# Kernel optimization log

Hardware: AMD Instinct MI355X
Metric: run time of the kernel (lower is better)

The kernel has to match this reference:

```python
import jax, jax.numpy as jnp
import numpy as np


def setup_inputs() -> dict:
    key = jax.random.key(0)
    kq, kk, kv = jax.random.split(key, 3)
    B, Lq, Lk, D = 4, 4096, 4096, 64
    return {
        "Q": jax.random.normal(kq, (B, Lq, D), dtype=jnp.float32),
        "K": jax.random.normal(kk, (B, Lk, D), dtype=jnp.float32),
        "V": jax.random.normal(kv, (B, Lk, D), dtype=jnp.float32),
    }


def reference(Q, K, V):
    # scores: [B, Lq, Lk]  (no 1/sqrt(d) scaling in the original module)
    scores = jnp.einsum("bqd,bkd->bqk", Q, K)
    attn = jax.nn.softmax(scores, axis=-1)
    # output: [B, Lq, D]
    return jnp.einsum("bqk,bkd->bqd", attn, V)
```

## Files before the change

### kernel.cpp

```cpp
#include <hip/hip_runtime.h>
#include <cmath>


#define B_    4
#define LQ    4096
#define LK    4096
#define DH    64
#define BQ    128
#define NQT2  (B_ * LQ / BQ)
#define NKVT  (LK / 128)
#define NROWS (B_ * LQ)
#define LOG2E 1.44269504088896f
#define C0    63.4785817991f

typedef _Float16 f16x8 __attribute__((ext_vector_type(8)));
typedef _Float16 f16x4 __attribute__((ext_vector_type(4)));
typedef float    f32x4 __attribute__((ext_vector_type(4)));
typedef short    s16x8 __attribute__((ext_vector_type(8)));
typedef int      i32x4 __attribute__((ext_vector_type(4)));

__device__ inline float exp2_(float x) {
#if __has_builtin(__builtin_amdgcn_exp2f)
  return __builtin_amdgcn_exp2f(x);
#else
  return exp2f(x);
#endif
}

__device__ inline unsigned pkbf16(float lo, float hi) {
  return __builtin_amdgcn_perm(__float_as_uint(hi), __float_as_uint(lo),
                               0x07060302u);
}

__device__ inline unsigned short bf16rne(float f) {
  unsigned u = __float_as_uint(f);
  return (unsigned short)((u + 0x7FFF + ((u >> 16) & 1)) >> 16);
}

__device__ inline void async16(const void* g, void* l) {
  __builtin_amdgcn_global_load_lds(
      (const __attribute__((address_space(1))) unsigned int*)g,
      (__attribute__((address_space(3))) unsigned int*)l, 16, 0, 0);
}

__global__ __launch_bounds__(256) void convert_kv8(
    const float* __restrict__ K, const float* __restrict__ V,
    const float* __restrict__ Q, _Float16* __restrict__ Kh,
    unsigned short* __restrict__ Vb, _Float16* __restrict__ Qh) {
  __shared__ unsigned short Vs[64 * 68];
  const int tid = threadIdx.x;
  const int bb = blockIdx.x;

  if (bb < 256) {
    const int b = bb >> 6, tile = (bb >> 1) & 31, half = bb & 1;
    const int kv0 = tile * 128 + half * 64;
    for (int i = 0; i < 2; ++i) {
      int q = i * 256 + tid;
      int r = q >> 3, g = q & 7;
      const float* src = K + ((size_t)(b * LK + kv0 + r)) * DH + g * 8;
      float4 a = *(const float4*)src;
      float4 d = *(const float4*)(src + 4);
      f16x8 hv = {(_Float16)(a.x * LOG2E), (_Float16)(a.y * LOG2E),
                  (_Float16)(a.z * LOG2E), (_Float16)(a.w * LOG2E),
                  (_Float16)(d.x * LOG2E), (_Float16)(d.y * LOG2E),
                  (_Float16)(d.z * LOG2E), (_Float16)(d.w * LOG2E)};
      int gp = g ^ (r & 7);
      size_t dst = ((size_t)(b * 32 + tile) * 128 + half * 64 + r) * 64 + gp * 8;
      *(f16x8*)(&Kh[dst]) = hv;
    }
  } else if (bb < 512) {
    const int cc = bb - 256;
    const int b = cc >> 6, tile = (cc >> 1) & 31, half = cc & 1;
    const int kv0 = tile * 128 + half * 64;
    for (int i = 0; i < 4; ++i) {
      int idx = i * 256 + tid;
      int vr = idx >> 4, c4 = idx & 15;
      float4 v = *(const float4*)(&V[((size_t)(b * LK + kv0 + vr)) * DH + c4 * 4]);
      Vs[vr * 68 + c4 * 4 + 0] = bf16rne(v.x);
      Vs[vr * 68 + c4 * 4 + 1] = bf16rne(v.y);
      Vs[vr * 68 + c4 * 4 + 2] = bf16rne(v.z);
      Vs[vr * 68 + c4 * 4 + 3] = bf16rne(v.w);
    }
    __syncthreads();
    for (int i = 0; i < 2; ++i) {
      int q = i * 256 + tid;
      int d = q >> 3, gl = q & 7;
      int g = half * 8 + gl;
      unsigned short ov[8];
#pragma unroll
      for (int j = 0; j < 8; ++j) {
        int p = g * 8 + j;
        int c = p >> 5, w5 = p & 31;
        int qd = w5 >> 3, jj = w5 & 7, hh = jj >> 2, r = jj & 3;
        int sL = 32 * c + 16 * hh + 4 * qd + r - 64 * half;
        ov[j] = Vs[sL * 68 + d];
      }
      int gp = g ^ (d & 7);
      size_t dst = ((size_t)(b * 32 + tile) * 64 + d) * 128 + gp * 8;
      s16x8 o8;
#pragma unroll
      for (int j = 0; j < 8; ++j) o8[j] = (short)ov[j];
      *(s16x8*)(&Vb[dst]) = o8;
    }
  } else {
    const int u = bb - 512;
    for (int i = 0; i < 4; ++i) {
      int idx = i * 256 + tid;
      int r = idx >> 4, c4 = idx & 15;
      size_t off = ((size_t)u * 64 + r) * DH + c4 * 4;
      float4 v = *(const float4*)(&Q[off]);
      f16x4 h = {(_Float16)v.x, (_Float16)v.y, (_Float16)v.z, (_Float16)v.w};
      *(f16x4*)(&Qh[off]) = h;
    }
  }
}

__global__ __launch_bounds__(256, 4) void ca_flash8(
    const _Float16* __restrict__ Qh, const _Float16* __restrict__ Kh,
    const unsigned short* __restrict__ Vb, float* __restrict__ Out,
    _Float16* __restrict__ Opart, float* __restrict__ Lw, int nsplit) {
  __shared__ _Float16 KsH[128 * 64];
  __shared__ unsigned short VtH[64 * 128];

  const int tid  = threadIdx.x;
  const int wave = tid >> 6;
  const int lane = tid & 63;
  const int quad = lane >> 4;
  const int l16  = lane & 15;
  const int e    = quad ^ (l16 & 7);

  const int qt    = blockIdx.x;
  const int b     = qt >> 5;
  const int qbase = (qt & 31) * BQ;
  const int sp    = blockIdx.y;
  const int t0 = (NKVT * sp) / nsplit;
  const int t1 = (NKVT * (sp + 1)) / nsplit;

  f16x8 qf[2][2];
#pragma unroll
  for (int sub = 0; sub < 2; ++sub) {
    int qrow = qbase + wave * 32 + sub * 16 + l16;
    const _Float16* qp = Qh + ((size_t)b * LQ + qrow) * DH + quad * 8;
#pragma unroll
    for (int kk = 0; kk < 2; ++kk)
      qf[sub][kk] = *(const f16x8*)(qp + kk * 32);
  }

  f32x4 o[2][5];
#pragma unroll
  for (int sub = 0; sub < 2; ++sub)
#pragma unroll
    for (int td = 0; td < 5; ++td) o[sub][td] = (f32x4){0.f, 0.f, 0.f, 0.f};

  s16x8 ones;
#pragma unroll
  for (int j = 0; j < 8; ++j) ones[j] = (short)0x3F80;

  const char* kg = (const char*)Kh + ((size_t)(b * 32 + t0)) * 16384;
  const char* vg = (const char*)Vb + ((size_t)(b * 32 + t0)) * 16384;
  char* ksB = (char*)KsH;
  char* vtB = (char*)VtH;
  const char* kR = ksB + l16 * 128;
  const char* vR = vtB + l16 * 256;

  for (int tile = t0; tile < t1; ++tile) {
    __syncthreads();
    const char* sg = (wave < 2) ? (kg + wave * 8192) : (vg + (wave - 2) * 8192);
    char*       sd = (wave < 2) ? (ksB + wave * 8192) : (vtB + (wave - 2) * 8192);
#pragma unroll
    for (int i = 0; i < 8; ++i) async16(sg + i * 1024 + lane * 16, sd + i * 1024);
    __syncthreads();
    kg += 16384; vg += 16384;

#pragma unroll
    for (int c = 0; c < 4; ++c) {
      f32x4 sv[2][2];
#pragma unroll
      for (int sub = 0; sub < 2; ++sub)
#pragma unroll
        for (int tt = 0; tt < 2; ++tt)
          sv[sub][tt] = (f32x4){-C0, -C0, -C0, -C0};
#pragma unroll
      for (int kk = 0; kk < 2; ++kk) {
        int ko = (e ^ (4 * kk)) * 16;
#pragma unroll
        for (int tt = 0; tt < 2; ++tt) {
          f16x8 bk = *(const f16x8*)(kR + (2 * c + tt) * 2048 + ko);
          sv[0][tt] = __builtin_amdgcn_mfma_f32_16x16x32_f16(bk, qf[0][kk], sv[0][tt], 0, 0, 0);
          sv[1][tt] = __builtin_amdgcn_mfma_f32_16x16x32_f16(bk, qf[1][kk], sv[1][tt], 0, 0, 0);
        }
      }

      s16x8 ap[2];
#pragma unroll
      for (int sub = 0; sub < 2; ++sub) {
        unsigned u0 = pkbf16(exp2_(sv[sub][0][0]), exp2_(sv[sub][0][1]));
        unsigned u1 = pkbf16(exp2_(sv[sub][0][2]), exp2_(sv[sub][0][3]));
        unsigned u2 = pkbf16(exp2_(sv[sub][1][0]), exp2_(sv[sub][1][1]));
        unsigned u3 = pkbf16(exp2_(sv[sub][1][2]), exp2_(sv[sub][1][3]));
        i32x4 iv = {(int)u0, (int)u1, (int)u2, (int)u3};
        ap[sub] = __builtin_bit_cast(s16x8, iv);
      }

      int vo = (e ^ (4 * c)) * 16;
#pragma unroll
      for (int td = 0; td < 4; ++td) {
        s16x8 bv = *(const s16x8*)(vR + td * 4096 + vo);
        o[0][td] = __builtin_amdgcn_mfma_f32_16x16x32_bf16(ap[0], bv, o[0][td], 0, 0, 0);
        o[1][td] = __builtin_amdgcn_mfma_f32_16x16x32_bf16(ap[1], bv, o[1][td], 0, 0, 0);
      }
      o[0][4] = __builtin_amdgcn_mfma_f32_16x16x32_bf16(ap[0], ones, o[0][4], 0, 0, 0);
      o[1][4] = __builtin_amdgcn_mfma_f32_16x16x32_bf16(ap[1], ones, o[1][4], 0, 0, 0);
    }
  }

  if (nsplit == 1) {
#pragma unroll
    for (int sub = 0; sub < 2; ++sub)
#pragma unroll
      for (int r = 0; r < 4; ++r) {
        float inv = 1.0f / (o[sub][4][r] + 1e-35f);
        size_t row = (size_t)b * LQ + qbase + wave * 32 + sub * 16 + quad * 4 + r;
#pragma unroll
        for (int td = 0; td < 4; ++td)
          Out[row * DH + td * 16 + l16] = o[sub][td][r] * inv;
      }
    return;
  }

#pragma unroll
  for (int sub = 0; sub < 2; ++sub)
#pragma unroll
    for (int r = 0; r < 4; ++r) {
      float l = o[sub][4][r];
      float inv = 1.0f / (l + 1e-35f);
      size_t g = (size_t)qt * BQ + wave * 32 + sub * 16 + quad * 4 + r;
      size_t prow = (size_t)sp * NROWS + g;
#pragma unroll
      for (int td = 0; td < 4; ++td)
        Opart[prow * DH + td * 16 + l16] = (_Float16)(o[sub][td][r] * inv);
      if (l16 == 0) Lw[prow] = l;
    }
}

__global__ __launch_bounds__(256) void ca_combine8(
    const _Float16* __restrict__ Opart, const float* __restrict__ Lw,
    float* __restrict__ Out, int nsplit) {
  const int idx = blockIdx.x * 256 + threadIdx.x;
  const int g = idx >> 4;
  const int c0 = (idx & 15) * 4;
  float den = 1e-30f;
  float a0 = 0.f, a1 = 0.f, a2 = 0.f, a3 = 0.f;
  for (int s = 0; s < nsplit; ++s) {
    size_t prow = (size_t)s * NROWS + g;
    float w = Lw[prow];
    f16x4 v = *(const f16x4*)(&Opart[prow * DH + c0]);
    a0 += w * (float)v[0]; a1 += w * (float)v[1];
    a2 += w * (float)v[2]; a3 += w * (float)v[3];
    den += w;
  }
  float inv = 1.0f / den;
  float4 ov = {a0 * inv, a1 * inv, a2 * inv, a3 * inv};
  *(float4*)(&Out[(size_t)g * DH + c0]) = ov;
}

#define LDSS 72
__global__ __launch_bounds__(256) void ca_flash_naive(
    const float* __restrict__ Q, const float* __restrict__ K,
    const float* __restrict__ V, float* __restrict__ Out) {
  __shared__ _Float16 Qs[64 * LDSS];
  __shared__ _Float16 Ks[64 * LDSS];
  __shared__ _Float16 Vt[64 * LDSS];
  __shared__ _Float16 Ps[64 * LDSS];
  const int tid = threadIdx.x, wave = tid >> 6, lane = tid & 63;
  const int quad = lane >> 4, l16 = lane & 15;
  const int b = blockIdx.x >> 6, qbase = (blockIdx.x & 63) * 64;
  for (int i = 0; i < 4; ++i) {
    int idx = (i * 256 + tid) * 4;
    int r = idx >> 6, c = idx & 63;
    float4 q4 = *(const float4*)(&Q[((size_t)b * LQ + qbase + r) * DH + c]);
    f16x4 hh = {(_Float16)q4.x, (_Float16)q4.y, (_Float16)q4.z, (_Float16)q4.w};
    *(f16x4*)(&Qs[r * LDSS + c]) = hh;
  }
  __syncthreads();
  f16x8 qf[2];
  qf[0] = *(const f16x8*)(&Qs[(wave * 16 + l16) * LDSS + quad * 8]);
  qf[1] = *(const f16x8*)(&Qs[(wave * 16 + l16) * LDSS + quad * 8 + 32]);
  float m_i[4], l_i[4];
  f32x4 o[4];
  for (int r = 0; r < 4; ++r) {
    m_i[r] = -INFINITY; l_i[r] = 0.f; o[r] = (f32x4){0.f, 0.f, 0.f, 0.f};
  }
  for (int kv0 = 0; kv0 < LK; kv0 += 64) {
    __syncthreads();
    for (int i = 0; i < 4; ++i) {
      int idx = (i * 256 + tid) * 4;
      int r = idx >> 6, c = idx & 63;
      float4 k4 = *(const float4*)(&K[((size_t)b * LK + kv0 + r) * DH + c]);
      f16x4 hh = {(_Float16)k4.x, (_Float16)k4.y, (_Float16)k4.z, (_Float16)k4.w};
      *(f16x4*)(&Ks[r * LDSS + c]) = hh;
      float4 v4 = *(const float4*)(&V[((size_t)b * LK + kv0 + r) * DH + c]);
      Vt[(c + 0) * LDSS + r] = (_Float16)v4.x;
      Vt[(c + 1) * LDSS + r] = (_Float16)v4.y;
      Vt[(c + 2) * LDSS + r] = (_Float16)v4.z;
      Vt[(c + 3) * LDSS + r] = (_Float16)v4.w;
    }
    __syncthreads();
    f32x4 sv[4];
    for (int t = 0; t < 4; ++t) sv[t] = (f32x4){0.f, 0.f, 0.f, 0.f};
    for (int kk = 0; kk < 2; ++kk)
      for (int t = 0; t < 4; ++t) {
        f16x8 bk = *(const f16x8*)(&Ks[(t * 16 + l16) * LDSS + quad * 8 + kk * 32]);
        sv[t] = __builtin_amdgcn_mfma_f32_16x16x32_f16(qf[kk], bk, sv[t], 0, 0, 0);
      }
    for (int r = 0; r < 4; ++r) {
      float mx = fmaxf(fmaxf(sv[0][r], sv[1][r]), fmaxf(sv[2][r], sv[3][r]));
      for (int off = 1; off < 16; off <<= 1) mx = fmaxf(mx, __shfl_xor(mx, off, 64));
      float mnew = fmaxf(m_i[r], mx);
      float alpha = __expf(m_i[r] - mnew);
      float rs = 0.f;
      for (int t = 0; t < 4; ++t) { float p = __expf(sv[t][r] - mnew); sv[t][r] = p; rs += p; }
      for (int off = 1; off < 16; off <<= 1) rs += __shfl_xor(rs, off, 64);
      l_i[r] = l_i[r] * alpha + rs;
      m_i[r] = mnew;
      for (int td = 0; td < 4; ++td) o[td][r] *= alpha;
    }
    for (int t = 0; t < 4; ++t)
      for (int r = 0; r < 4; ++r)
        Ps[(wave * 16 + quad * 4 + r) * LDSS + t * 16 + l16] = (_Float16)sv[t][r];
    for (int kk = 0; kk < 2; ++kk) {
      f16x8 ap = *(const f16x8*)(&Ps[(wave * 16 + l16) * LDSS + quad * 8 + kk * 32]);
      for (int td = 0; td < 4; ++td) {
        f16x8 bv = *(const f16x8*)(&Vt[(td * 16 + l16) * LDSS + quad * 8 + kk * 32]);
        o[td] = __builtin_amdgcn_mfma_f32_16x16x32_f16(ap, bv, o[td], 0, 0, 0);
      }
    }
  }
  float inv_l[4];
  for (int r = 0; r < 4; ++r) inv_l[r] = 1.0f / l_i[r];
  for (int td = 0; td < 4; ++td)
    for (int r = 0; r < 4; ++r) {
      size_t row = (size_t)b * LQ + qbase + wave * 16 + quad * 4 + r;
      Out[row * DH + td * 16 + l16] = o[td][r] * inv_l[r];
    }
}

extern "C" void kernel_launch(void* const* d_in, const int* in_sizes, int n_in,
                              void* d_out, int out_size, void* d_ws, size_t ws_size,
                              hipStream_t stream) {
  const float* Q = (const float*)d_in[0];
  const float* K = (const float*)d_in[1];
  const float* V = (const float*)d_in[2];
  float* Out = (float*)d_out;

  const size_t sKh = (size_t)B_ * LK * DH * sizeof(_Float16);
  const size_t sVb = (size_t)B_ * LK * DH * sizeof(unsigned short);
  const size_t sQh = (size_t)NROWS * DH * sizeof(_Float16);
  const size_t base = sKh + sVb + sQh;
  auto opSize = [](int sp) { return (size_t)sp * NROWS * DH * sizeof(_Float16); };
  auto lwSize = [](int sp) { return (size_t)sp * NROWS * sizeof(float); };

  int split = 0;
  if (base + opSize(8) + lwSize(8) <= ws_size) split = 8;
  else if (base + opSize(4) + lwSize(4) <= ws_size) split = 4;
  else if (base + opSize(2) + lwSize(2) <= ws_size) split = 2;
  else if (base <= ws_size) split = 1;

  char* ws = (char*)d_ws;
  if (split >= 1) {
    _Float16* Kh = (_Float16*)ws;
    unsigned short* Vb = (unsigned short*)(ws + sKh);
    _Float16* Qh = (_Float16*)(ws + sKh + sVb);
    convert_kv8<<<dim3(768), dim3(256), 0, stream>>>(K, V, Q, Kh, Vb, Qh);
    if (split == 1) {
      ca_flash8<<<dim3(NQT2, 1), dim3(256), 0, stream>>>(
          Qh, Kh, Vb, Out, nullptr, nullptr, 1);
    } else {
      _Float16* Op = (_Float16*)(ws + base);
      float* Lwp = (float*)(ws + base + opSize(split));
      ca_flash8<<<dim3(NQT2, split), dim3(256), 0, stream>>>(
          Qh, Kh, Vb, Out, Op, Lwp, split);
      ca_combine8<<<dim3(NROWS * DH / 4 / 256), dim3(256), 0, stream>>>(
          Op, Lwp, Out, split);
    }
  } else {
    ca_flash_naive<<<dim3(256), dim3(256), 0, stream>>>(Q, K, V, Out);
  }
}
```

Baseline: 94.02 us.

## Double query tile per block to 256 rows for more K/V reuse

Each wave now handles 64 query rows (four 16-row sub-tiles) instead of 32, so every K/V tile staged in LDS feeds twice as many MFMAs. This halves the global-to-LDS traffic and the barrier count per query row. The cost is roughly double the accumulator and Q-fragment registers, with the occupancy hint lowered from 4 to 2 blocks per CU. With split 8 the grid shrinks from 1024 to 512 blocks, which may underfill the GPU.

Result: no change. 95.08 us (+1.1%).

```diff
diff --git a/kernel.cpp b/kernel.cpp
--- a/kernel.cpp
+++ b/kernel.cpp
@@ -6,8 +6,8 @@
 #define LQ    4096
 #define LK    4096
 #define DH    64
-#define BQ    128
-#define NQT2  (B_ * LQ / BQ)
+#define BQ    256
+#define NQT3  (B_ * LQ / BQ)
 #define NKVT  (LK / 128)
 #define NROWS (B_ * LQ)
 #define LOG2E 1.44269504088896f
@@ -115,7 +115,7 @@
   }
 }
 
-__global__ __launch_bounds__(256, 4) void ca_flash8(
+__global__ __launch_bounds__(256, 2) void ca_flash9(
     const _Float16* __restrict__ Qh, const _Float16* __restrict__ Kh,
     const unsigned short* __restrict__ Vb, float* __restrict__ Out,
     _Float16* __restrict__ Opart, float* __restrict__ Lw, int nsplit) {
@@ -130,25 +130,25 @@
   const int e    = quad ^ (l16 & 7);
 
   const int qt    = blockIdx.x;
-  const int b     = qt >> 5;
-  const int qbase = (qt & 31) * BQ;
+  const int b     = qt >> 4;
+  const int qbase = (qt & 15) * BQ;
   const int sp    = blockIdx.y;
   const int t0 = (NKVT * sp) / nsplit;
   const int t1 = (NKVT * (sp + 1)) / nsplit;
 
-  f16x8 qf[2][2];
-#pragma unroll
-  for (int sub = 0; sub < 2; ++sub) {
-    int qrow = qbase + wave * 32 + sub * 16 + l16;
+  f16x8 qf[4][2];
+#pragma unroll
+  for (int sub = 0; sub < 4; ++sub) {
+    int qrow = qbase + wave * 64 + sub * 16 + l16;
     const _Float16* qp = Qh + ((size_t)b * LQ + qrow) * DH + quad * 8;
 #pragma unroll
     for (int kk = 0; kk < 2; ++kk)
       qf[sub][kk] = *(const f16x8*)(qp + kk * 32);
   }
 
-  f32x4 o[2][5];
-#pragma unroll
-  for (int sub = 0; sub < 2; ++sub)
+  f32x4 o[4][5];
+#pragma unroll
+  for (int sub = 0; sub < 4; ++sub)
 #pragma unroll
     for (int td = 0; td < 5; ++td) o[sub][td] = (f32x4){0.f, 0.f, 0.f, 0.f};
 
@@ -174,9 +174,9 @@
 
 #pragma unroll
     for (int c = 0; c < 4; ++c) {
-      f32x4 sv[2][2];
-#pragma unroll
-      for (int sub = 0; sub < 2; ++sub)
+      f32x4 sv[4][2];
+#pragma unroll
+      for (int sub = 0; sub < 4; ++sub)
 #pragma unroll
         for (int tt = 0; tt < 2; ++tt)
           sv[sub][tt] = (f32x4){-C0, -C0, -C0, -C0};
@@ -186,14 +186,16 @@
 #pragma unroll
         for (int tt = 0; tt < 2; ++tt) {
           f16x8 bk = *(const f16x8*)(kR + (2 * c + tt) * 2048 + ko);
-          sv[0][tt] = __builtin_amdgcn_mfma_f32_16x16x32_f16(bk, qf[0][kk], sv[0][tt], 0, 0, 0);
-          sv[1][tt] = __builtin_amdgcn_mfma_f32_16x16x32_f16(bk, qf[1][kk], sv[1][tt], 0, 0, 0);
+#pragma unroll
+          for (int sub = 0; sub < 4; ++sub)
+            sv[sub][tt] = __builtin_amdgcn_mfma_f32_16x16x32_f16(
+                bk, qf[sub][kk], sv[sub][tt], 0, 0, 0);
         }
       }
 
-      s16x8 ap[2];
-#pragma unroll
-      for (int sub = 0; sub < 2; ++sub) {
+      s16x8 ap[4];
+#pragma unroll
+      for (int sub = 0; sub < 4; ++sub) {
         unsigned u0 = pkbf16(exp2_(sv[sub][0][0]), exp2_(sv[sub][0][1]));
         unsigned u1 = pkbf16(exp2_(sv[sub][0][2]), exp2_(sv[sub][0][3]));
         unsigned u2 = pkbf16(exp2_(sv[sub][1][0]), exp2_(sv[sub][1][1]));
@@ -206,21 +208,25 @@
 #pragma unroll
       for (int td = 0; td < 4; ++td) {
         s16x8 bv = *(const s16x8*)(vR + td * 4096 + vo);
-        o[0][td] = __builtin_amdgcn_mfma_f32_16x16x32_bf16(ap[0], bv, o[0][td], 0, 0, 0);
-        o[1][td] = __builtin_amdgcn_mfma_f32_16x16x32_bf16(ap[1], bv, o[1][td], 0, 0, 0);
-      }
-      o[0][4] = __builtin_amdgcn_mfma_f32_16x16x32_bf16(ap[0], ones, o[0][4], 0, 0, 0);
-      o[1][4] = __builtin_amdgcn_mfma_f32_16x16x32_bf16(ap[1], ones, o[1][4], 0, 0, 0);
+#pragma unroll
+        for (int sub = 0; sub < 4; ++sub)
+          o[sub][td] = __builtin_amdgcn_mfma_f32_16x16x32_bf16(
+              ap[sub], bv, o[sub][td], 0, 0, 0);
+      }
+#pragma unroll
+      for (int sub = 0; sub < 4; ++sub)
+        o[sub][4] = __builtin_amdgcn_mfma_f32_16x16x32_bf16(
+            ap[sub], ones, o[sub][4], 0, 0, 0);
     }
   }
 
   if (nsplit == 1) {
 #pragma unroll
-    for (int sub = 0; sub < 2; ++sub)
+    for (int sub = 0; sub < 4; ++sub)
 #pragma unroll
       for (int r = 0; r < 4; ++r) {
         float inv = 1.0f / (o[sub][4][r] + 1e-35f);
-        size_t row = (size_t)b * LQ + qbase + wave * 32 + sub * 16 + quad * 4 + r;
+        size_t row = (size_t)b * LQ + qbase + wave * 64 + sub * 16 + quad * 4 + r;
 #pragma unroll
         for (int td = 0; td < 4; ++td)
           Out[row * DH + td * 16 + l16] = o[sub][td][r] * inv;
@@ -229,12 +235,12 @@
   }
 
 #pragma unroll
-  for (int sub = 0; sub < 2; ++sub)
+  for (int sub = 0; sub < 4; ++sub)
 #pragma unroll
     for (int r = 0; r < 4; ++r) {
       float l = o[sub][4][r];
       float inv = 1.0f / (l + 1e-35f);
-      size_t g = (size_t)qt * BQ + wave * 32 + sub * 16 + quad * 4 + r;
+      size_t g = (size_t)qt * BQ + wave * 64 + sub * 16 + quad * 4 + r;
       size_t prow = (size_t)sp * NROWS + g;
 #pragma unroll
       for (int td = 0; td < 4; ++td)
@@ -243,7 +249,7 @@
     }
 }
 
-__global__ __launch_bounds__(256) void ca_combine8(
+__global__ __launch_bounds__(256) void ca_combine9(
     const _Float16* __restrict__ Opart, const float* __restrict__ Lw,
     float* __restrict__ Out, int nsplit) {
   const int idx = blockIdx.x * 256 + threadIdx.x;
@@ -373,14 +379,14 @@
     _Float16* Qh = (_Float16*)(ws + sKh + sVb);
     convert_kv8<<<dim3(768), dim3(256), 0, stream>>>(K, V, Q, Kh, Vb, Qh);
     if (split == 1) {
-      ca_flash8<<<dim3(NQT2, 1), dim3(256), 0, stream>>>(
+      ca_flash9<<<dim3(NQT3, 1), dim3(256), 0, stream>>>(
           Qh, Kh, Vb, Out, nullptr, nullptr, 1);
     } else {
       _Float16* Op = (_Float16*)(ws + base);
       float* Lwp = (float*)(ws + base + opSize(split));
-      ca_flash8<<<dim3(NQT2, split), dim3(256), 0, stream>>>(
+      ca_flash9<<<dim3(NQT3, split), dim3(256), 0, stream>>>(
           Qh, Kh, Vb, Out, Op, Lwp, split);
-      ca_combine8<<<dim3(NROWS * DH / 4 / 256), dim3(256), 0, stream>>>(
+      ca_combine9<<<dim3(NROWS * DH / 4 / 256), dim3(256), 0, stream>>>(
           Op, Lwp, Out, split);
     }
   } else {
```
